# Performance work log

Hardware: AMD Instinct MI355X
Metric: run time of the kernel (lower is better)

The kernel has to match this reference:

```python
import jax, jax.numpy as jnp
import numpy as np

N_NODES = 131072   # total nodes across all ego-graphs
B = 16384          # number of graphs (ego nodes)
N_PER = N_NODES // B  # nodes per graph (uniform for the synthetic batch)
IN_CH = 1024
OUT_CH = 512
NUM_CENTERS = 16


def setup_inputs() -> dict:
    key = jax.random.key(0)
    k1, k2, k3, k4 = jax.random.split(key, 4)
    gnn_x = jax.random.normal(k1, (N_NODES, IN_CH), dtype=jnp.float32)
    Wc = jax.random.normal(k2, (NUM_CENTERS, IN_CH), dtype=jnp.float32) * (IN_CH ** -0.5)
    W_experts = jax.random.normal(k3, (NUM_CENTERS, OUT_CH, IN_CH), dtype=jnp.float32) * (IN_CH ** -0.5)
    # sorted segment ids: graph g owns nodes [g*N_PER, (g+1)*N_PER)
    batch = (jnp.arange(N_NODES) // N_PER).astype(jnp.int64)
    # ego node offset within each graph
    ego_idx = jax.random.randint(k4, (B,), 0, N_PER).astype(jnp.int64)
    return {"gnn_x": gnn_x, "Wc": Wc, "W_experts": W_experts, "batch": batch, "ego_idx": ego_idx}


def reference(gnn_x, Wc, W_experts, batch, ego_idx):
    # get_ds_x: first node index of each graph (diff_idxs) + per-graph ego offset
    n_graphs = ego_idx.shape[0]
    starts = jnp.searchsorted(batch, jnp.arange(n_graphs, dtype=batch.dtype))  # [B]
    ego_idxs = starts + ego_idx                                               # [B]
    ds_x = gnn_x[ego_idxs]                                                    # [B, in]

    # route each ego embedding to one of num_centers experts via argmax
    center_scores = ds_x @ Wc.T                 # [B, num_centers]
    center_idx = jnp.argmax(center_scores, axis=1)  # [B]

    # per-node expert linear: logits[b] = W_experts[center_idx[b]] @ ds_x[b]
    W_sel = W_experts[center_idx]               # [B, out, in]
    logits = jnp.einsum('bi,boi->bo', ds_x, W_sel)  # [B, out]
    return logits
```

## Files before the change

### kernel.cpp

```cpp
#include <hip/hip_runtime.h>
#include <hip/hip_bf16.h>
#include <stdint.h>

#define N_NODES_C 131072
#define B_C       16384
#define IN_C      1024
#define OUT_C     512
#define NC_C      16

typedef short s16x8 __attribute__((ext_vector_type(8)));
typedef float f32x4 __attribute__((ext_vector_type(4)));

__device__ __forceinline__ unsigned short f2bf(float f) {
  union { float f; unsigned u; } v; v.f = f;
  unsigned u = v.u;
  unsigned r = (u + 0x7fffu + ((u >> 16) & 1u)) >> 16;
  return (unsigned short)r;
}

__device__ __forceinline__ void async_cp16(void* lds, const void* g) {
  __builtin_amdgcn_global_load_lds(
      (const __attribute__((address_space(1))) unsigned int*)g,
      (__attribute__((address_space(3))) unsigned int*)lds, 16, 0, 0);
}

__device__ __forceinline__ float dpp_reduce_add(float x) {
  float t;
  t = __int_as_float(__builtin_amdgcn_update_dpp(0, __float_as_int(x), 0x111, 0xf, 0xf, false)); x += t;
  t = __int_as_float(__builtin_amdgcn_update_dpp(0, __float_as_int(x), 0x112, 0xf, 0xf, false)); x += t;
  t = __int_as_float(__builtin_amdgcn_update_dpp(0, __float_as_int(x), 0x114, 0xf, 0xf, false)); x += t;
  t = __int_as_float(__builtin_amdgcn_update_dpp(0, __float_as_int(x), 0x118, 0xf, 0xf, false)); x += t;
  t = __int_as_float(__builtin_amdgcn_update_dpp(0, __float_as_int(x), 0x142, 0xa, 0xf, false)); x += t;
  t = __int_as_float(__builtin_amdgcn_update_dpp(0, __float_as_int(x), 0x143, 0xc, 0xf, false)); x += t;
  return x;
}

__global__ __launch_bounds__(512) void k_fused(
    const float* __restrict__ W, unsigned short* __restrict__ Wb,
    const float* __restrict__ gnn_x, const float* __restrict__ Wc,
    const int* __restrict__ batch, const int* __restrict__ ego_idx,
    unsigned short* __restrict__ xb, int* __restrict__ rows_sorted,
    int* __restrict__ cursors) {
  const int bid = blockIdx.x;
  const int t = threadIdx.x;

  if (bid >= 512) {
    const int i = ((bid - 512) * 512 + t) * 4;
    float4 v = *(const float4*)&W[i];
    ushort4 h;
    h.x = f2bf(v.x); h.y = f2bf(v.y); h.z = f2bf(v.z); h.w = f2bf(v.w);
    *(ushort4*)&Wb[i] = h;
    return;
  }

  __shared__ float wc[NC_C * IN_C];
  __shared__ int sbest[32];
  __shared__ int sbase[16];

  for (int i = t * 4; i < NC_C * IN_C; i += 512 * 4)
    *(float4*)&wc[i] = *(const float4*)&Wc[i];
  __syncthreads();

  const int w = t >> 6, l = t & 63;
  const int gbase = bid * 32;
  const int gw = gbase + w * 4;

  const int gq = gw + (l & 3);
  int lo = 0, hi = N_NODES_C;
  while (lo < hi) { int mid = (lo + hi) >> 1; if (batch[mid] < gq) lo = mid + 1; else hi = mid; }
  const int srcq = lo + ego_idx[gq];

  #pragma unroll
  for (int pp = 0; pp < 2; ++pp) {
    float4 xv[2][4];
    #pragma unroll
    for (int rr = 0; rr < 2; ++rr) {
      const int src_row = __shfl(srcq, pp * 2 + rr, 64);
      const float* xp = gnn_x + (size_t)src_row * IN_C;
      #pragma unroll
      for (int j = 0; j < 4; ++j) xv[rr][j] = *(const float4*)&xp[j * 256 + l * 4];
      unsigned short* dst = &xb[(size_t)(gw + pp * 2 + rr) * IN_C];
      #pragma unroll
      for (int j = 0; j < 4; ++j) {
        ushort4 h;
        h.x = f2bf(xv[rr][j].x); h.y = f2bf(xv[rr][j].y);
        h.z = f2bf(xv[rr][j].z); h.w = f2bf(xv[rr][j].w);
        *(ushort4*)&dst[j * 256 + l * 4] = h;
      }
    }

    float bv0 = -1e38f, bv1 = -1e38f;
    int best0 = 0, best1 = 0;
    #pragma unroll
    for (int c = 0; c < NC_C; ++c) {
      float a0 = 0.f, a1 = 0.f;
      #pragma unroll
      for (int j = 0; j < 4; ++j) {
        float4 wv = *(const float4*)&wc[c * IN_C + j * 256 + l * 4];
        a0 += xv[0][j].x * wv.x + xv[0][j].y * wv.y + xv[0][j].z * wv.z + xv[0][j].w * wv.w;
        a1 += xv[1][j].x * wv.x + xv[1][j].y * wv.y + xv[1][j].z * wv.z + xv[1][j].w * wv.w;
      }
      a0 = dpp_reduce_add(a0);
      a1 = dpp_reduce_add(a1);
      if (a0 > bv0) { bv0 = a0; best0 = c; }
      if (a1 > bv1) { bv1 = a1; best1 = c; }
    }
    if (l == 63) {
      sbest[w * 4 + pp * 2]     = best0;
      sbest[w * 4 + pp * 2 + 1] = best1;
    }
  }

  __syncthreads();
  if (t < 16) {
    int n = 0;
    #pragma unroll
    for (int r = 0; r < 32; ++r) n += (sbest[r] == t);
    if (n) sbase[t] = atomicAdd(&cursors[t * 16], n);
  }
  __syncthreads();
  if (t < 32) {
    const int c = sbest[t];
    int rank = 0;
    for (int r = 0; r < t; ++r) rank += (sbest[r] == c);
    rows_sorted[c * B_C + sbase[c] + rank] = gbase + t;
  }
}

__global__ __launch_bounds__(512) void k_gemm(
    const unsigned short* __restrict__ xb, const unsigned short* __restrict__ Wb,
    const int* __restrict__ rows_sorted, const int* __restrict__ cnts,
    float* __restrict__ out) {
  const int i = blockIdx.x + 4 * blockIdx.y + 512 * blockIdx.z;
  const int xcd = i & 7;
  const int j = i >> 3;
  const int e = xcd * 2 + (j & 1);
  const int r = j >> 1;
  const int mt = r >> 2;
  const int nt = r & 3;

  const int cnt = cnts[e * 16];
  const int m0 = mt * 128;
  if (m0 >= cnt) return;
  const int n0 = nt * 128;

  __shared__ unsigned short Al[2][128 * 64];
  __shared__ unsigned short Bl[2][128 * 64];

  const int t = threadIdx.x;
  const int w = t >> 6, l = t & 63;

  const int srow = t >> 3;
  const int scolb = (t & 7) * 16;
  const char* bbase = (const char*)Wb + ((size_t)e * OUT_C + n0) * (IN_C * 2);
  const char* aptr[2];
  const char* bptr[2];
  #pragma unroll
  for (int ii = 0; ii < 2; ++ii) {
    const int row = srow + ii * 64;
    const int sw = scolb ^ ((row & 7) << 4);
    const int p = m0 + row;
    const int rid = (p < cnt) ? rows_sorted[e * B_C + p] : 0;
    aptr[ii] = (const char*)xb + (size_t)rid * (IN_C * 2) + sw;
    bptr[ii] = bbase + (size_t)row * (IN_C * 2) + sw;
  }

  const f32x4 fz = {0.f, 0.f, 0.f, 0.f};
  f32x4 acc[2][4];
  #pragma unroll
  for (int mi = 0; mi < 2; ++mi)
    #pragma unroll
    for (int ni = 0; ni < 4; ++ni) acc[mi][ni] = fz;

#define STAGE(buf, kt) do {                                        \
    char* ab_ = (char*)&Al[buf][0] + w * 1024;                     \
    char* bb_ = (char*)&Bl[buf][0] + w * 1024;                     \
    const size_t ko_ = (size_t)(kt) * 128;                         \
    _Pragma("unroll")                                              \
    for (int i_ = 0; i_ < 2; ++i_) {                               \
      async_cp16(ab_ + i_ * 8192, aptr[i_] + ko_);                 \
      async_cp16(bb_ + i_ * 8192, bptr[i_] + ko_);                 \
    }                                                              \
  } while (0)

  STAGE(0, 0);
  __syncthreads();

  const int wm = w >> 1, wn = w & 1;
  const int lrow = l & 15, kg = l >> 4;
  const int NKT = IN_C / 64;

  int cur = 0;
  for (int kt = 0; kt < NKT; ++kt) {
    if (kt + 1 < NKT) STAGE(cur ^ 1, kt + 1);
    #pragma unroll
    for (int ks = 0; ks < 2; ++ks) {
      const int cb = ks * 64 + kg * 16;
      s16x8 a[2], b[4];
      #pragma unroll
      for (int mi = 0; mi < 2; ++mi) {
        const int row = wm * 32 + mi * 16 + lrow;
        a[mi] = *(const s16x8*)((const char*)&Al[cur][0] + row * 128 + (cb ^ ((row & 7) << 4)));
      }
      #pragma unroll
      for (int ni = 0; ni < 4; ++ni) {
        const int row = wn * 64 + ni * 16 + lrow;
        b[ni] = *(const s16x8*)((const char*)&Bl[cur][0] + row * 128 + (cb ^ ((row & 7) << 4)));
      }
      #pragma unroll
      for (int mi = 0; mi < 2; ++mi)
        #pragma unroll
        for (int ni = 0; ni < 4; ++ni)
          acc[mi][ni] = __builtin_amdgcn_mfma_f32_16x16x32_bf16(a[mi], b[ni], acc[mi][ni], 0, 0, 0);
    }
    __syncthreads();
    cur ^= 1;
  }
#undef STAGE

  #pragma unroll
  for (int mi = 0; mi < 2; ++mi) {
    #pragma unroll
    for (int reg = 0; reg < 4; ++reg) {
      const int p = m0 + wm * 32 + mi * 16 + kg * 4 + reg;
      if (p < cnt) {
        const int rid = rows_sorted[e * B_C + p];
        float* orow = out + (size_t)rid * OUT_C + n0 + wn * 64 + lrow;
        #pragma unroll
        for (int ni = 0; ni < 4; ++ni) orow[ni * 16] = acc[mi][ni][reg];
      }
    }
  }
}

extern "C" void kernel_launch(void* const* d_in, const int* in_sizes, int n_in,
                              void* d_out, int out_size, void* d_ws, size_t ws_size,
                              hipStream_t stream) {
  const float* gnn_x     = (const float*)d_in[0];
  const float* Wc        = (const float*)d_in[1];
  const float* W_experts = (const float*)d_in[2];
  const int*   batch     = (const int*)d_in[3];
  const int*   ego_idx   = (const int*)d_in[4];
  float* out = (float*)d_out;

  uint8_t* ws = (uint8_t*)d_ws;
  unsigned short* xb     = (unsigned short*)ws;
  unsigned short* W_bf16 = (unsigned short*)(ws + 33554432);
  int* rows_sorted = (int*)(ws + 50331648);
  int* cursors     = (int*)(ws + 51380224);

  hipMemsetAsync(cursors, 0, NC_C * 16 * sizeof(int), stream);
  k_fused<<<dim3(512 + 4096), dim3(512), 0, stream>>>(W_experts, W_bf16, gnn_x, Wc,
                                                      batch, ego_idx, xb, rows_sorted, cursors);
  k_gemm<<<dim3(OUT_C / 128, B_C / 128, NC_C), dim3(512), 0, stream>>>(xb, W_bf16, rows_sorted, cursors, out);
}
```

Measured before the change: 80.66 us.

## Make expert GEMM persistent with smaller 128x64 tiles and 32-wide K steps

Replaces the 3D grid of 128x128 tiles with a persistent 1024-block grid that loops over virtual tiles of 128x64, skipping tiles that lie beyond each expert's row count. The K step is halved to 32, which shrinks the LDS footprint and allows more blocks per CU. Per-expert counts are cached in shared memory once per block. The aim is to cut the launch cost of many empty blocks and to balance work across CUs. In exchange, arithmetic intensity per tile drops, W is re-read more often, and each K step now needs a barrier, so synchronisation happens twice as often.

```diff
diff --git a/kernel.cpp b/kernel.cpp
--- a/kernel.cpp
+++ b/kernel.cpp
@@ -131,103 +131,94 @@
     const unsigned short* __restrict__ xb, const unsigned short* __restrict__ Wb,
     const int* __restrict__ rows_sorted, const int* __restrict__ cnts,
     float* __restrict__ out) {
-  const int i = blockIdx.x + 4 * blockIdx.y + 512 * blockIdx.z;
-  const int xcd = i & 7;
-  const int j = i >> 3;
-  const int e = xcd * 2 + (j & 1);
-  const int r = j >> 1;
-  const int mt = r >> 2;
-  const int nt = r & 3;
-
-  const int cnt = cnts[e * 16];
-  const int m0 = mt * 128;
-  if (m0 >= cnt) return;
-  const int n0 = nt * 128;
-
-  __shared__ unsigned short Al[2][128 * 64];
-  __shared__ unsigned short Bl[2][128 * 64];
+  __shared__ unsigned short Al[2][128 * 32];
+  __shared__ unsigned short Bl[2][64 * 32];
+  __shared__ int cn_s[16];
 
   const int t = threadIdx.x;
   const int w = t >> 6, l = t & 63;
 
-  const int srow = t >> 3;
-  const int scolb = (t & 7) * 16;
-  const char* bbase = (const char*)Wb + ((size_t)e * OUT_C + n0) * (IN_C * 2);
-  const char* aptr[2];
-  const char* bptr[2];
-  #pragma unroll
-  for (int ii = 0; ii < 2; ++ii) {
-    const int row = srow + ii * 64;
-    const int sw = scolb ^ ((row & 7) << 4);
-    const int p = m0 + row;
-    const int rid = (p < cnt) ? rows_sorted[e * B_C + p] : 0;
-    aptr[ii] = (const char*)xb + (size_t)rid * (IN_C * 2) + sw;
-    bptr[ii] = bbase + (size_t)row * (IN_C * 2) + sw;
-  }
-
-  const f32x4 fz = {0.f, 0.f, 0.f, 0.f};
-  f32x4 acc[2][4];
-  #pragma unroll
-  for (int mi = 0; mi < 2; ++mi)
-    #pragma unroll
-    for (int ni = 0; ni < 4; ++ni) acc[mi][ni] = fz;
-
-#define STAGE(buf, kt) do {                                        \
-    char* ab_ = (char*)&Al[buf][0] + w * 1024;                     \
-    char* bb_ = (char*)&Bl[buf][0] + w * 1024;                     \
-    const size_t ko_ = (size_t)(kt) * 128;                         \
-    _Pragma("unroll")                                              \
-    for (int i_ = 0; i_ < 2; ++i_) {                               \
-      async_cp16(ab_ + i_ * 8192, aptr[i_] + ko_);                 \
-      async_cp16(bb_ + i_ * 8192, bptr[i_] + ko_);                 \
-    }                                                              \
-  } while (0)
-
-  STAGE(0, 0);
-  __syncthreads();
+  if (t < 16) cn_s[t] = cnts[t * 16];
+  __syncthreads();
+
+  const int srow = t >> 2;
+  const int scolb = (t & 3) * 16;
+  const int ssw = scolb ^ ((srow & 3) << 4);
 
   const int wm = w >> 1, wn = w & 1;
   const int lrow = l & 15, kg = l >> 4;
-  const int NKT = IN_C / 64;
-
-  int cur = 0;
-  for (int kt = 0; kt < NKT; ++kt) {
-    if (kt + 1 < NKT) STAGE(cur ^ 1, kt + 1);
-    #pragma unroll
-    for (int ks = 0; ks < 2; ++ks) {
-      const int cb = ks * 64 + kg * 16;
-      s16x8 a[2], b[4];
+  const int cb = kg * 16;
+
+  for (int vi = blockIdx.x; vi < 16384; vi += 1024) {
+    const int j = vi >> 3;
+    const int e = (vi & 7) * 2 + (j & 1);
+    const int r = j >> 1;
+    const int mt = r >> 3;
+    const int nt = r & 7;
+
+    const int cnt = cn_s[e];
+    const int m0 = mt * 128;
+    if (m0 >= cnt) continue;
+    const int n0 = nt * 64;
+
+    const int p = m0 + srow;
+    const int rid = (p < cnt) ? rows_sorted[e * B_C + p] : 0;
+    const char* aptr = (const char*)xb + (size_t)rid * (IN_C * 2) + ssw;
+    const char* bptr = (const char*)Wb + ((size_t)e * OUT_C + n0 + srow) * (IN_C * 2) + ssw;
+
+    const f32x4 fz = {0.f, 0.f, 0.f, 0.f};
+    f32x4 acc[2][2];
+    #pragma unroll
+    for (int mi = 0; mi < 2; ++mi)
+      #pragma unroll
+      for (int ni = 0; ni < 2; ++ni) acc[mi][ni] = fz;
+
+#define STAGE(buf, kt) do {                                         \
+    async_cp16((char*)&Al[buf][0] + w * 1024, aptr + (size_t)(kt) * 64); \
+    if (t < 256) async_cp16((char*)&Bl[buf][0] + w * 1024, bptr + (size_t)(kt) * 64); \
+  } while (0)
+
+    STAGE(0, 0);
+    __syncthreads();
+
+    int cur = 0;
+    const int NKT = IN_C / 32;
+    for (int kt = 0; kt < NKT; ++kt) {
+      if (kt + 1 < NKT) STAGE(cur ^ 1, kt + 1);
+      const char* Ab = (const char*)&Al[cur][0];
+      const char* Bb = (const char*)&Bl[cur][0];
+      s16x8 a[2], b[2];
       #pragma unroll
       for (int mi = 0; mi < 2; ++mi) {
         const int row = wm * 32 + mi * 16 + lrow;
-        a[mi] = *(const s16x8*)((const char*)&Al[cur][0] + row * 128 + (cb ^ ((row & 7) << 4)));
-      }
-      #pragma unroll
-      for (int ni = 0; ni < 4; ++ni) {
-        const int row = wn * 64 + ni * 16 + lrow;
-        b[ni] = *(const s16x8*)((const char*)&Bl[cur][0] + row * 128 + (cb ^ ((row & 7) << 4)));
+        a[mi] = *(const s16x8*)(Ab + row * 64 + (cb ^ ((row & 3) << 4)));
+      }
+      #pragma unroll
+      for (int ni = 0; ni < 2; ++ni) {
+        const int row = wn * 32 + ni * 16 + lrow;
+        b[ni] = *(const s16x8*)(Bb + row * 64 + (cb ^ ((row & 3) << 4)));
       }
       #pragma unroll
       for (int mi = 0; mi < 2; ++mi)
         #pragma unroll
-        for (int ni = 0; ni < 4; ++ni)
+        for (int ni = 0; ni < 2; ++ni)
           acc[mi][ni] = __builtin_amdgcn_mfma_f32_16x16x32_bf16(a[mi], b[ni], acc[mi][ni], 0, 0, 0);
-    }
-    __syncthreads();
-    cur ^= 1;
-  }
+      __syncthreads();
+      cur ^= 1;
+    }
 #undef STAGE
 
-  #pragma unroll
-  for (int mi = 0; mi < 2; ++mi) {
-    #pragma unroll
-    for (int reg = 0; reg < 4; ++reg) {
-      const int p = m0 + wm * 32 + mi * 16 + kg * 4 + reg;
-      if (p < cnt) {
-        const int rid = rows_sorted[e * B_C + p];
-        float* orow = out + (size_t)rid * OUT_C + n0 + wn * 64 + lrow;
-        #pragma unroll
-        for (int ni = 0; ni < 4; ++ni) orow[ni * 16] = acc[mi][ni][reg];
+    #pragma unroll
+    for (int mi = 0; mi < 2; ++mi) {
+      #pragma unroll
+      for (int reg = 0; reg < 4; ++reg) {
+        const int pp = m0 + wm * 32 + mi * 16 + kg * 4 + reg;
+        if (pp < cnt) {
+          const int orid = rows_sorted[e * B_C + pp];
+          float* orow = out + (size_t)orid * OUT_C + n0 + wn * 32 + lrow;
+          #pragma unroll
+          for (int ni = 0; ni < 2; ++ni) orow[ni * 16] = acc[mi][ni][reg];
+        }
       }
     }
   }
@@ -252,5 +243,5 @@
   hipMemsetAsync(cursors, 0, NC_C * 16 * sizeof(int), stream);
   k_fused<<<dim3(512 + 4096), dim3(512), 0, stream>>>(W_experts, W_bf16, gnn_x, Wc,
                                                       batch, ego_idx, xb, rows_sorted, cursors);
-  k_gemm<<<dim3(OUT_C / 128, B_C / 128, NC_C), dim3(512), 0, stream>>>(xb, W_bf16, rows_sorted, cursors, out);
-}
+  k_gemm<<<dim3(1024), dim3(512), 0, stream>>>(xb, W_bf16, rows_sorted, cursors, out);
+}
```

New measurement: 84.74 us. +5.1%, slower.
